# Optimization experiments

Hardware: AMD Instinct MI355X
Metric: run time of the kernel (lower is better)

## Reference

```python
import jax, jax.numpy as jnp
import numpy as np

B, T, D = 2, 2048, 2048
Q_HEADS, KV_HEADS, HEAD_DIM = 16, 4, 128
ROPE_BASE = 10000.0


def _apply_rotary(x_nhd, positions_n):
    # x_nhd: (N, H, head_dim); half-split rotary embedding.
    half = x_nhd.shape[-1] // 2
    inv_freq = 1.0 / (ROPE_BASE ** (jnp.arange(half, dtype=jnp.float32) / half))
    ang = positions_n.astype(jnp.float32)[:, None] * inv_freq  # (N, half)
    cos = jnp.cos(ang)[:, None, :]  # (N, 1, half)
    sin = jnp.sin(ang)[:, None, :]
    x1, x2 = x_nhd[..., :half], x_nhd[..., half:]
    return jnp.concatenate([x1 * cos - x2 * sin, x1 * sin + x2 * cos], axis=-1)


def setup_inputs() -> dict:
    key = jax.random.key(0)
    ks = jax.random.split(key, 5)
    s_in = 1.0 / np.sqrt(D)
    s_o = 1.0 / np.sqrt(Q_HEADS * HEAD_DIM)
    x = jax.random.normal(ks[0], (B, T, D), dtype=jnp.float32)
    positions = jnp.broadcast_to(jnp.arange(T, dtype=jnp.int32), (B, T))
    wq = jax.random.normal(ks[1], (Q_HEADS * HEAD_DIM, D), dtype=jnp.float32) * s_in
    wk = jax.random.normal(ks[2], (KV_HEADS * HEAD_DIM, D), dtype=jnp.float32) * s_in
    wv = jax.random.normal(ks[3], (KV_HEADS * HEAD_DIM, D), dtype=jnp.float32) * s_in
    wo = jax.random.normal(ks[4], (D, Q_HEADS * HEAD_DIM), dtype=jnp.float32) * s_o
    return {"x": x, "positions": positions, "wq": wq, "wk": wk, "wv": wv, "wo": wo}


def reference(x, positions, wq, wk, wv, wo):
    bsz, tsz, _ = x.shape
    q = jnp.einsum('btd,od->bto', x, wq).reshape(bsz, tsz, Q_HEADS, HEAD_DIM)
    k = jnp.einsum('btd,od->bto', x, wk).reshape(bsz, tsz, KV_HEADS, HEAD_DIM)
    v = jnp.einsum('btd,od->bto', x, wv).reshape(bsz, tsz, KV_HEADS, HEAD_DIM)
    pos_flat = positions.reshape(-1)
    q = _apply_rotary(q.reshape(-1, Q_HEADS, HEAD_DIM), pos_flat).reshape(bsz, tsz, Q_HEADS, HEAD_DIM)
    k = _apply_rotary(k.reshape(-1, KV_HEADS, HEAD_DIM), pos_flat).reshape(bsz, tsz, KV_HEADS, HEAD_DIM)
    rep = Q_HEADS // KV_HEADS
    k = jnp.repeat(k, rep, axis=2)
    v = jnp.repeat(v, rep, axis=2)
    logits = jnp.einsum('bthd,bThd->bhtT', q, k) / jnp.sqrt(jnp.float32(HEAD_DIM))
    causal = jnp.tril(jnp.ones((tsz, tsz), dtype=bool))
    logits = jnp.where(causal[None, None], logits, -1e9)
    weights = jax.nn.softmax(logits, axis=-1)
    ctx = jnp.einsum('bhtT,bThd->bthd', weights, v).reshape(bsz, tsz, Q_HEADS * HEAD_DIM)
    return jnp.einsum('bto,do->btd', ctx, wo)
```

## Files before the change

### kernel.cpp

```cpp
#include <hip/hip_runtime.h>
#include <hip/hip_bf16.h>

typedef __bf16 bf16x8 __attribute__((ext_vector_type(8)));
typedef float  f32x4  __attribute__((ext_vector_type(4)));
typedef float  f32x16 __attribute__((ext_vector_type(16)));
typedef unsigned int u32x2 __attribute__((ext_vector_type(2)));

#define B_   2
#define T_   2048
#define D_   2048
#define QH_  16
#define KVH_ 4
#define HD_  128
#define BT_  (B_ * T_)
#define KVD_ 512
#define SCL  0.12751744f

#define GLOAD_LDS16(g, l)                                        \
  __builtin_amdgcn_global_load_lds(                              \
      (const __attribute__((address_space(1))) void*)(g),        \
      (__attribute__((address_space(3))) void*)(l), 16, 0, 0)

#define SWZ(row)  ((((row) >> 3) ^ (row)) & 15)
#define SWZ8(row) ((((row) >> 3) ^ (row)) & 7)

__global__ __launch_bounds__(256) void cvt_all(
    const float* __restrict__ x, const float* __restrict__ wq,
    const float* __restrict__ wk, const float* __restrict__ wv,
    const float* __restrict__ wo, ushort* __restrict__ out) {
  const int i = blockIdx.x * 256 + threadIdx.x;
  int j = i;
  const float* src;
  float mul = 1.f;
  if (j < 2097152) { src = x; }
  else if ((j -= 2097152) < 1048576) { src = wq; mul = SCL; }
  else if ((j -= 1048576) < 262144)  { src = wk; }
  else if ((j -= 262144) < 262144)   { src = wv; }
  else { j -= 262144; src = wo; }
  float4 v = ((const float4*)src)[j];
  __hip_bfloat16 h0 = __float2bfloat16(v.x * mul);
  __hip_bfloat16 h1 = __float2bfloat16(v.y * mul);
  __hip_bfloat16 h2 = __float2bfloat16(v.z * mul);
  __hip_bfloat16 h3 = __float2bfloat16(v.w * mul);
  ushort4 o;
  o.x = *(ushort*)&h0; o.y = *(ushort*)&h1;
  o.z = *(ushort*)&h2; o.w = *(ushort*)&h3;
  ((ushort4*)out)[i] = o;
}

__global__ __launch_bounds__(256) void gemm_qkv(
    const ushort* __restrict__ X, const ushort* __restrict__ WQ,
    const ushort* __restrict__ WK, const ushort* __restrict__ WV,
    ushort* __restrict__ qo, ushort* __restrict__ ko, ushort* __restrict__ vo) {
  const int nb = blockIdx.x % 24;
  const int mb = blockIdx.x / 24;
  const int tid = threadIdx.x;
  const int wave = tid >> 6;
  const int lane = tid & 63;
  const int mrow = lane & 15;
  const int quad = lane >> 4;
  const int wm = wave >> 1;
  const int wn = wave & 1;
  const int m0 = mb * 128;
  const int K = D_;

  const ushort* Wg;
  if (nb < 16)      Wg = WQ + (size_t)nb * 128 * K;
  else if (nb < 20) Wg = WK + (size_t)(nb - 16) * 128 * K;
  else              Wg = WV + (size_t)(nb - 20) * 128 * K;

  __shared__ __align__(16) ushort At[2][128 * 64];
  __shared__ __align__(16) ushort Bt[2][128 * 64];

  f32x4 acc[4][4];
#pragma unroll
  for (int i = 0; i < 4; ++i)
#pragma unroll
    for (int j = 0; j < 4; ++j) acc[i][j] = (f32x4){0.f, 0.f, 0.f, 0.f};

  const ushort* Xg = X + (size_t)m0 * K;

  auto STAGE = [&](int buf, int k0) {
#pragma unroll
    for (int p = 0; p < 4; ++p) {
      const int c = p * 256 + tid;
      const int row = c >> 3;
      const int cc = (c & 7) ^ (row & 7);
      GLOAD_LDS16(Xg + (size_t)row * K + k0 + cc * 8,
                  At[buf] + (size_t)(p * 256 + wave * 64) * 8);
      GLOAD_LDS16(Wg + (size_t)row * K + k0 + cc * 8,
                  Bt[buf] + (size_t)(p * 256 + wave * 64) * 8);
    }
  };

  const int NT = K / 64;
  STAGE(0, 0);
  STAGE(1, 64);

  for (int t = 0; t < NT; ++t) {
    const int cur = t & 1;
    if (t + 2 < NT) asm volatile("s_waitcnt vmcnt(8)" ::: "memory");
    else            asm volatile("s_waitcnt vmcnt(0)" ::: "memory");
    __builtin_amdgcn_s_barrier();

    const ushort* Ac = At[cur];
    const ushort* Bc = Bt[cur];
#pragma unroll
    for (int s = 0; s < 2; ++s) {
      bf16x8 af[4], bfr[4];
#pragma unroll
      for (int mt = 0; mt < 4; ++mt) {
        const int row = wm * 64 + mt * 16 + mrow;
        af[mt] = *reinterpret_cast<const bf16x8*>(
            Ac + row * 64 + (((s * 4 + quad) ^ (row & 7)) * 8));
      }
#pragma unroll
      for (int nt = 0; nt < 4; ++nt) {
        const int row = wn * 64 + nt * 16 + mrow;
        bfr[nt] = *reinterpret_cast<const bf16x8*>(
            Bc + row * 64 + (((s * 4 + quad) ^ (row & 7)) * 8));
      }
#pragma unroll
      for (int mt = 0; mt < 4; ++mt)
#pragma unroll
        for (int nt = 0; nt < 4; ++nt)
          acc[mt][nt] = __builtin_amdgcn_mfma_f32_16x16x32_bf16(
              af[mt], bfr[nt], acc[mt][nt], 0, 0, 0);
    }

    asm volatile("s_waitcnt lgkmcnt(0)" ::: "memory");
    __builtin_amdgcn_s_barrier();
    if (t + 2 < NT) STAGE(cur, (t + 2) * 64);
  }

#pragma unroll
  for (int mt = 0; mt < 4; ++mt) {
#pragma unroll
    for (int nt = 0; nt < 4; ++nt) {
      const int colw = wn * 64 + nt * 16 + mrow;
      const int row0 = m0 + wm * 64 + mt * 16 + quad * 4;
      if (nb < 16) {
        const int col = nb * 128 + colw;
#pragma unroll
        for (int r = 0; r < 4; ++r) {
          __hip_bfloat16 hh = __float2bfloat16(acc[mt][nt][r]);
          qo[(size_t)(row0 + r) * 2048 + col] = *(ushort*)&hh;
        }
      } else if (nb < 20) {
        const int col = (nb - 16) * 128 + colw;
#pragma unroll
        for (int r = 0; r < 4; ++r) {
          __hip_bfloat16 hh = __float2bfloat16(acc[mt][nt][r]);
          ko[(size_t)(row0 + r) * KVD_ + col] = *(ushort*)&hh;
        }
      } else {
        const int col = (nb - 20) * 128 + colw;
        const int bb = row0 >> 11;
        const int t0 = row0 & (T_ - 1);
        ushort4 s4;
#pragma unroll
        for (int r = 0; r < 4; ++r) {
          __hip_bfloat16 hh = __float2bfloat16(acc[mt][nt][r]);
          (&s4.x)[r] = *(ushort*)&hh;
        }
        *(ushort4*)(vo + ((size_t)(bb * KVD_ + col)) * T_ + t0) = s4;
      }
    }
  }
}

__global__ __launch_bounds__(256) void gemm_o(
    const ushort* __restrict__ X, const ushort* __restrict__ W,
    float* __restrict__ Y, int M, int N, int K) {
  const int nb128 = N >> 7;
  const int mb = blockIdx.x / nb128;
  const int nb = blockIdx.x % nb128;
  const int tid = threadIdx.x;
  const int wave = tid >> 6;
  const int lane = tid & 63;
  const int mrow = lane & 15;
  const int quad = lane >> 4;
  const int wm = wave >> 1;
  const int wn = wave & 1;
  const int m0 = mb * 128;
  const int n0 = nb * 128;

  __shared__ __align__(16) ushort At[2][128 * 64];
  __shared__ __align__(16) ushort Bt[2][128 * 64];

  f32x4 acc[4][4];
#pragma unroll
  for (int i = 0; i < 4; ++i)
#pragma unroll
    for (int j = 0; j < 4; ++j) acc[i][j] = (f32x4){0.f, 0.f, 0.f, 0.f};

  const ushort* Xg = X + (size_t)m0 * K;
  const ushort* Wg = W + (size_t)n0 * K;

  auto STAGE = [&](int buf, int k0) {
#pragma unroll
    for (int p = 0; p < 4; ++p) {
      const int c = p * 256 + tid;
      const int row = c >> 3;
      const int cc = (c & 7) ^ (row & 7);
      GLOAD_LDS16(Xg + (size_t)row * K + k0 + cc * 8,
                  At[buf] + (size_t)(p * 256 + wave * 64) * 8);
      GLOAD_LDS16(Wg + (size_t)row * K + k0 + cc * 8,
                  Bt[buf] + (size_t)(p * 256 + wave * 64) * 8);
    }
  };

  const int NT = K / 64;
  STAGE(0, 0);
  STAGE(1, 64);

  for (int t = 0; t < NT; ++t) {
    const int cur = t & 1;
    if (t + 2 < NT) asm volatile("s_waitcnt vmcnt(8)" ::: "memory");
    else            asm volatile("s_waitcnt vmcnt(0)" ::: "memory");
    __builtin_amdgcn_s_barrier();

    const ushort* Ac = At[cur];
    const ushort* Bc = Bt[cur];
#pragma unroll
    for (int s = 0; s < 2; ++s) {
      bf16x8 af[4], bfr[4];
#pragma unroll
      for (int mt = 0; mt < 4; ++mt) {
        const int row = wm * 64 + mt * 16 + mrow;
        af[mt] = *reinterpret_cast<const bf16x8*>(
            Ac + row * 64 + (((s * 4 + quad) ^ (row & 7)) * 8));
      }
#pragma unroll
      for (int nt = 0; nt < 4; ++nt) {
        const int row = wn * 64 + nt * 16 + mrow;
        bfr[nt] = *reinterpret_cast<const bf16x8*>(
            Bc + row * 64 + (((s * 4 + quad) ^ (row & 7)) * 8));
      }
#pragma unroll
      for (int mt = 0; mt < 4; ++mt)
#pragma unroll
        for (int nt = 0; nt < 4; ++nt)
          acc[mt][nt] = __builtin_amdgcn_mfma_f32_16x16x32_bf16(
              af[mt], bfr[nt], acc[mt][nt], 0, 0, 0);
    }

    asm volatile("s_waitcnt lgkmcnt(0)" ::: "memory");
    __builtin_amdgcn_s_barrier();
    if (t + 2 < NT) STAGE(cur, (t + 2) * 64);
  }

#pragma unroll
  for (int mt = 0; mt < 4; ++mt)
#pragma unroll
    for (int nt = 0; nt < 4; ++nt) {
      const int col = n0 + wn * 64 + nt * 16 + mrow;
      const int row0 = m0 + wm * 64 + mt * 16 + quad * 4;
#pragma unroll
      for (int r = 0; r < 4; ++r)
        Y[(size_t)(row0 + r) * N + col] = acc[mt][nt][r];
    }
}

__global__ __launch_bounds__(256) void rope_kernel(
    __hip_bfloat16* __restrict__ q, __hip_bfloat16* __restrict__ k,
    const int* __restrict__ positions) {
  const int wave = threadIdx.x >> 6;
  const int lane = threadIdx.x & 63;
  const int p = blockIdx.x * 4 + wave;
  const int head = p % (QH_ + KVH_);
  const int bt = p / (QH_ + KVH_);

  __hip_bfloat16* base;
  if (head < QH_) base = q + ((size_t)bt * QH_ + head) * HD_;
  else            base = k + ((size_t)bt * KVH_ + (head - QH_)) * HD_;

  const float pos = (float)positions[bt];
  const float inv_freq = exp2f((float)lane * -0.20762050593f);
  const float ang = pos * inv_freq;
  const float c = cosf(ang);
  const float s = sinf(ang);

  const float x1 = __bfloat162float(base[lane]);
  const float x2 = __bfloat162float(base[lane + 64]);
  base[lane]      = __float2bfloat16(x1 * c - x2 * s);
  base[lane + 64] = __float2bfloat16(x1 * s + x2 * c);
}

static __device__ __forceinline__ unsigned pk2(float a, float b) {
  __hip_bfloat16 ha = __float2bfloat16(a);
  __hip_bfloat16 hb = __float2bfloat16(b);
  return (unsigned)(*(ushort*)&ha) | ((unsigned)(*(ushort*)&hb) << 16);
}

static __device__ __forceinline__ void hswap(unsigned& a, unsigned& b,
                                             const int hi) {
#if __has_builtin(__builtin_amdgcn_permlane32_swap)
  u32x2 r = __builtin_amdgcn_permlane32_swap(a, b, false, false);
  a = r.x;
  b = r.y;
#else
  unsigned s = __shfl_xor(hi ? a : b, 32, 64);
  unsigned na = hi ? s : a;
  b = hi ? b : s;
  a = na;
#endif
}

__global__ __launch_bounds__(256, 2) void attn_mfma(
    const ushort* __restrict__ q, const ushort* __restrict__ k,
    const ushort* __restrict__ vt, ushort* __restrict__ ctx) {
  const int tid = threadIdx.x;
  const int wave = tid >> 6;
  const int lane = tid & 63;
  const int m5 = lane & 31;
  const int hi = lane >> 5;
  const int parity = wave & 1;
  const int hh = wave >> 1;

  const int i = blockIdx.x;
  const int qt = i & 63;
  const int g  = i >> 6;
  const int b   = g >> 3;
  const int hkv = (g >> 1) & 3;
  const int hp  = g & 1;
  const int hq  = hkv * 4 + hp * 2 + hh;
  const int q0  = qt * 32;

  __shared__ __align__(16) ushort smem[16384];
  __shared__ float lbuf[2][32];
  ushort* kt   = smem;
  ushort* vtl  = smem + 8192;

  const ushort* qrow =
      q + ((size_t)(b * T_ + q0 + m5) * QH_ + hq) * HD_ + hi * 8;
  bf16x8 qf[8];
#pragma unroll
  for (int c = 0; c < 8; ++c)
    qf[c] = *reinterpret_cast<const bf16x8*>(qrow + c * 16);

  f32x16 o4[4];
#pragma unroll
  for (int dt = 0; dt < 4; ++dt)
#pragma unroll
    for (int r = 0; r < 16; ++r) o4[dt][r] = 0.f;
  float ls = 0.f;

  const ushort* kbase = k + ((size_t)b * T_ * KVH_ + hkv) * HD_;
  const ushort* vbase = vt + (size_t)(b * KVD_ + hkv * HD_) * T_;

  const int ns = (qt >> 1) + 1;

  for (int s = 0; s < ns; ++s) {
    const int j0 = s * 64;

#pragma unroll
    for (int p = 0; p < 4; ++p) {
      const int c = p * 256 + tid;
      const int krow = c >> 4;
      const int kco = (c & 15) ^ SWZ(krow);
      GLOAD_LDS16(kbase + (size_t)(j0 + krow) * KVD_ + kco * 8,
                  kt + (size_t)(p * 256 + wave * 64) * 8);
    }
#pragma unroll
    for (int p = 0; p < 4; ++p) {
      const int c = p * 256 + tid;
      const int vrow = c >> 3;
      const int vco = (c & 7) ^ SWZ8(vrow);
      GLOAD_LDS16(vbase + (size_t)vrow * T_ + j0 + vco * 8,
                  vtl + (size_t)(p * 256 + wave * 64) * 8);
    }
    asm volatile("s_waitcnt vmcnt(4)" ::: "memory");
    __builtin_amdgcn_s_barrier();

    const int c32 = 2 * s + parity;
    unsigned u0, u1, u2, u3, u4, u5, u6, u7;

    if (c32 <= qt) {
      __builtin_amdgcn_s_setprio(1);
      f32x16 sa;
#pragma unroll
      for (int r = 0; r < 16; ++r) sa[r] = 0.f;
      const int rowk = parity * 32 + m5;
#pragma unroll
      for (int c = 0; c < 8; ++c) {
        const int ch = (2 * c + hi) ^ SWZ(rowk);
        bf16x8 kf = *reinterpret_cast<const bf16x8*>(kt + rowk * 128 + ch * 8);
        sa = __builtin_amdgcn_mfma_f32_32x32x16_bf16(kf, qf[c], sa, 0, 0, 0);
      }

      float p[16];
      if (c32 == qt) {
#pragma unroll
        for (int r = 0; r < 16; ++r) {
          const int roff = (r & 3) + 8 * (r >> 2) + 4 * hi;
          p[r] = (roff > m5) ? 0.f : exp2f(sa[r]);
        }
      } else {
#pragma unroll
        for (int r = 0; r < 16; ++r) p[r] = exp2f(sa[r]);
      }
#pragma unroll
      for (int r = 0; r < 16; ++r) ls += p[r];

      u0 = pk2(p[0], p[1]);   u1 = pk2(p[2], p[3]);
      u2 = pk2(p[4], p[5]);   u3 = pk2(p[6], p[7]);
      u4 = pk2(p[8], p[9]);   u5 = pk2(p[10], p[11]);
      u6 = pk2(p[12], p[13]); u7 = pk2(p[14], p[15]);
      hswap(u0, u2, hi); hswap(u1, u3, hi);
      hswap(u4, u6, hi); hswap(u5, u7, hi);
      __builtin_amdgcn_s_setprio(0);
    }

    asm volatile("s_waitcnt vmcnt(0)" ::: "memory");
    __builtin_amdgcn_s_barrier();

    if (c32 <= qt) {
      __builtin_amdgcn_s_setprio(1);
#pragma unroll
      for (int half = 0; half < 2; ++half) {
        union { unsigned w[4]; bf16x8 v; } pa;
        pa.w[0] = half ? u4 : u0;
        pa.w[1] = half ? u5 : u1;
        pa.w[2] = half ? u6 : u2;
        pa.w[3] = half ? u7 : u3;
        const int gc2 = parity * 4 + half * 2;
#pragma unroll
        for (int dt = 0; dt < 4; ++dt) {
          const int rowv = dt * 32 + m5;
          const int chv = (gc2 + hi) ^ SWZ8(rowv);
          bf16x8 vf =
              *reinterpret_cast<const bf16x8*>(vtl + rowv * 64 + chv * 8);
          o4[dt] = __builtin_amdgcn_mfma_f32_32x32x16_bf16(pa.v, vf, o4[dt],
                                                           0, 0, 0);
        }
      }
      __builtin_amdgcn_s_setprio(0);
    }

    asm volatile("s_waitcnt lgkmcnt(0)" ::: "memory");
    __builtin_amdgcn_s_barrier();
  }

  const float lt = ls + __shfl_xor(ls, 32, 64);
  float* sO = (float*)smem;
  if (parity) {
#pragma unroll
    for (int reg = 0; reg < 16; ++reg) {
      const int qrw = (reg & 3) + 8 * (reg >> 2) + 4 * hi;
#pragma unroll
      for (int dt = 0; dt < 4; ++dt)
        sO[hh * 4096 + qrw * 128 + dt * 32 + m5] = o4[dt][reg];
    }
    if (hi == 0) lbuf[hh][m5] = lt;
  }
  __syncthreads();
  if (!parity) {
    const float ltot = lt + lbuf[hh][m5];
#pragma unroll
    for (int reg = 0; reg < 16; ++reg) {
      const int qrw = (reg & 3) + 8 * (reg >> 2) + 4 * hi;
      const float rl = 1.f / __shfl(ltot, qrw, 64);
      ushort* op =
          ctx + ((size_t)(b * T_ + q0 + qrw) * QH_ + hq) * HD_ + m5;
#pragma unroll
      for (int dt = 0; dt < 4; ++dt) {
        const float ov = o4[dt][reg] + sO[hh * 4096 + qrw * 128 + dt * 32 + m5];
        __hip_bfloat16 hb = __float2bfloat16(ov * rl);
        op[dt * 32] = *(ushort*)&hb;
      }
    }
  }
}

extern "C" void kernel_launch(void* const* d_in, const int* in_sizes, int n_in,
                              void* d_out, int out_size, void* d_ws, size_t ws_size,
                              hipStream_t stream) {
  const float* x  = (const float*)d_in[0];
  const int* pos  = (const int*)d_in[1];
  const float* wq = (const float*)d_in[2];
  const float* wk = (const float*)d_in[3];
  const float* wv = (const float*)d_in[4];
  const float* wo = (const float*)d_in[5];

  ushort* xb  = (ushort*)d_ws;
  ushort* wqb = xb  + (size_t)8388608;
  ushort* wkb = wqb + (size_t)4194304;
  ushort* wvb = wkb + (size_t)1048576;
  ushort* wob = wvb + (size_t)1048576;
  ushort* qb  = wob + (size_t)4194304;
  ushort* kb  = qb  + (size_t)8388608;
  ushort* vtb = kb  + (size_t)2097152;
  ushort* ctx = xb;

  cvt_all<<<18432, 256, 0, stream>>>(x, wq, wk, wv, wo, (ushort*)d_ws);

  gemm_qkv<<<(BT_ / 128) * 24, 256, 0, stream>>>(xb, wqb, wkb, wvb, qb, kb, vtb);

  rope_kernel<<<(BT_ * (QH_ + KVH_)) / 4, 256, 0, stream>>>(
      (__hip_bfloat16*)qb, (__hip_bfloat16*)kb, pos);

  attn_mfma<<<1024, 256, 0, stream>>>(qb, kb, vtb, ctx);

  gemm_o<<<(BT_ / 128) * (D_ / 128), 256, 0, stream>>>(
      ctx, wob, (float*)d_out, BT_, D_, QH_ * HD_);
}
```

Before: 331.9 us.

## Pair causal query tiles per block and double-buffer K/V staging in attention

Each attention block now handles two query tiles, a long one (63-pj) and a short one (pj), so the causal work per block is balanced. The grid is halved to 512 blocks. K/V tiles are double-buffered in LDS so the next tile's global-to-LDS load overlaps compute on the current one. The wait before the P·V step is removed. LDS doubles to 64KB per block, which may reduce occupancy, and fewer blocks may underfill the GPU.

```diff
diff --git a/kernel.cpp b/kernel.cpp
--- a/kernel.cpp
+++ b/kernel.cpp
@@ -318,158 +318,167 @@
   const int parity = wave & 1;
   const int hh = wave >> 1;
 
-  const int i = blockIdx.x;
-  const int qt = i & 63;
-  const int g  = i >> 6;
+  const int pj = blockIdx.x & 31;
+  const int g  = blockIdx.x >> 5;
   const int b   = g >> 3;
   const int hkv = (g >> 1) & 3;
   const int hp  = g & 1;
   const int hq  = hkv * 4 + hp * 2 + hh;
-  const int q0  = qt * 32;
-
-  __shared__ __align__(16) ushort smem[16384];
+
+  __shared__ __align__(16) ushort smem[32768];
   __shared__ float lbuf[2][32];
-  ushort* kt   = smem;
-  ushort* vtl  = smem + 8192;
-
-  const ushort* qrow =
-      q + ((size_t)(b * T_ + q0 + m5) * QH_ + hq) * HD_ + hi * 8;
-  bf16x8 qf[8];
-#pragma unroll
-  for (int c = 0; c < 8; ++c)
-    qf[c] = *reinterpret_cast<const bf16x8*>(qrow + c * 16);
-
-  f32x16 o4[4];
-#pragma unroll
-  for (int dt = 0; dt < 4; ++dt)
-#pragma unroll
-    for (int r = 0; r < 16; ++r) o4[dt][r] = 0.f;
-  float ls = 0.f;
 
   const ushort* kbase = k + ((size_t)b * T_ * KVH_ + hkv) * HD_;
   const ushort* vbase = vt + (size_t)(b * KVD_ + hkv * HD_) * T_;
 
-  const int ns = (qt >> 1) + 1;
-
-  for (int s = 0; s < ns; ++s) {
-    const int j0 = s * 64;
-
-#pragma unroll
-    for (int p = 0; p < 4; ++p) {
-      const int c = p * 256 + tid;
-      const int krow = c >> 4;
-      const int kco = (c & 15) ^ SWZ(krow);
-      GLOAD_LDS16(kbase + (size_t)(j0 + krow) * KVD_ + kco * 8,
-                  kt + (size_t)(p * 256 + wave * 64) * 8);
-    }
-#pragma unroll
-    for (int p = 0; p < 4; ++p) {
-      const int c = p * 256 + tid;
-      const int vrow = c >> 3;
-      const int vco = (c & 7) ^ SWZ8(vrow);
-      GLOAD_LDS16(vbase + (size_t)vrow * T_ + j0 + vco * 8,
-                  vtl + (size_t)(p * 256 + wave * 64) * 8);
-    }
-    asm volatile("s_waitcnt vmcnt(4)" ::: "memory");
-    __builtin_amdgcn_s_barrier();
-
-    const int c32 = 2 * s + parity;
-    unsigned u0, u1, u2, u3, u4, u5, u6, u7;
-
-    if (c32 <= qt) {
-      __builtin_amdgcn_s_setprio(1);
-      f32x16 sa;
-#pragma unroll
-      for (int r = 0; r < 16; ++r) sa[r] = 0.f;
-      const int rowk = parity * 32 + m5;
-#pragma unroll
-      for (int c = 0; c < 8; ++c) {
-        const int ch = (2 * c + hi) ^ SWZ(rowk);
-        bf16x8 kf = *reinterpret_cast<const bf16x8*>(kt + rowk * 128 + ch * 8);
-        sa = __builtin_amdgcn_mfma_f32_32x32x16_bf16(kf, qf[c], sa, 0, 0, 0);
-      }
-
-      float p[16];
-      if (c32 == qt) {
-#pragma unroll
-        for (int r = 0; r < 16; ++r) {
-          const int roff = (r & 3) + 8 * (r >> 2) + 4 * hi;
-          p[r] = (roff > m5) ? 0.f : exp2f(sa[r]);
-        }
+  for (int job = 0; job < 2; ++job) {
+    const int qt = job ? pj : 63 - pj;
+    const int q0 = qt * 32;
+    const int ns = (qt >> 1) + 1;
+
+    const ushort* qrow =
+        q + ((size_t)(b * T_ + q0 + m5) * QH_ + hq) * HD_ + hi * 8;
+    bf16x8 qf[8];
+#pragma unroll
+    for (int c = 0; c < 8; ++c)
+      qf[c] = *reinterpret_cast<const bf16x8*>(qrow + c * 16);
+
+    f32x16 o4[4];
+#pragma unroll
+    for (int dt = 0; dt < 4; ++dt)
+#pragma unroll
+      for (int r = 0; r < 16; ++r) o4[dt][r] = 0.f;
+    float ls = 0.f;
+
+    auto STAGE = [&](int buf, int s) {
+      const int j0 = s * 64;
+      ushort* kb_ = smem + buf * 16384;
+      ushort* vb_ = smem + buf * 16384 + 8192;
+#pragma unroll
+      for (int p = 0; p < 4; ++p) {
+        const int c = p * 256 + tid;
+        const int krow = c >> 4;
+        const int kco = (c & 15) ^ SWZ(krow);
+        GLOAD_LDS16(kbase + (size_t)(j0 + krow) * KVD_ + kco * 8,
+                    kb_ + (size_t)(p * 256 + wave * 64) * 8);
+      }
+#pragma unroll
+      for (int p = 0; p < 4; ++p) {
+        const int c = p * 256 + tid;
+        const int vrow = c >> 3;
+        const int vco = (c & 7) ^ SWZ8(vrow);
+        GLOAD_LDS16(vbase + (size_t)vrow * T_ + j0 + vco * 8,
+                    vb_ + (size_t)(p * 256 + wave * 64) * 8);
+      }
+    };
+
+    STAGE(0, 0);
+
+    for (int s = 0; s < ns; ++s) {
+      const int cur = s & 1;
+      if (s + 1 < ns) {
+        STAGE(cur ^ 1, s + 1);
+        asm volatile("s_waitcnt vmcnt(8)" ::: "memory");
       } else {
-#pragma unroll
-        for (int r = 0; r < 16; ++r) p[r] = exp2f(sa[r]);
-      }
-#pragma unroll
-      for (int r = 0; r < 16; ++r) ls += p[r];
-
-      u0 = pk2(p[0], p[1]);   u1 = pk2(p[2], p[3]);
-      u2 = pk2(p[4], p[5]);   u3 = pk2(p[6], p[7]);
-      u4 = pk2(p[8], p[9]);   u5 = pk2(p[10], p[11]);
-      u6 = pk2(p[12], p[13]); u7 = pk2(p[14], p[15]);
-      hswap(u0, u2, hi); hswap(u1, u3, hi);
-      hswap(u4, u6, hi); hswap(u5, u7, hi);
-      __builtin_amdgcn_s_setprio(0);
-    }
-
-    asm volatile("s_waitcnt vmcnt(0)" ::: "memory");
-    __builtin_amdgcn_s_barrier();
-
-    if (c32 <= qt) {
-      __builtin_amdgcn_s_setprio(1);
-#pragma unroll
-      for (int half = 0; half < 2; ++half) {
-        union { unsigned w[4]; bf16x8 v; } pa;
-        pa.w[0] = half ? u4 : u0;
-        pa.w[1] = half ? u5 : u1;
-        pa.w[2] = half ? u6 : u2;
-        pa.w[3] = half ? u7 : u3;
-        const int gc2 = parity * 4 + half * 2;
+        asm volatile("s_waitcnt vmcnt(0)" ::: "memory");
+      }
+      __builtin_amdgcn_s_barrier();
+
+      const ushort* kt  = smem + cur * 16384;
+      const ushort* vtl = smem + cur * 16384 + 8192;
+      const int c32 = 2 * s + parity;
+
+      if (c32 <= qt) {
+        __builtin_amdgcn_s_setprio(1);
+        f32x16 sa;
+#pragma unroll
+        for (int r = 0; r < 16; ++r) sa[r] = 0.f;
+        const int rowk = parity * 32 + m5;
+#pragma unroll
+        for (int c = 0; c < 8; ++c) {
+          const int ch = (2 * c + hi) ^ SWZ(rowk);
+          bf16x8 kf =
+              *reinterpret_cast<const bf16x8*>(kt + rowk * 128 + ch * 8);
+          sa = __builtin_amdgcn_mfma_f32_32x32x16_bf16(kf, qf[c], sa, 0, 0, 0);
+        }
+
+        float p[16];
+        if (c32 == qt) {
+#pragma unroll
+          for (int r = 0; r < 16; ++r) {
+            const int roff = (r & 3) + 8 * (r >> 2) + 4 * hi;
+            p[r] = (roff > m5) ? 0.f : exp2f(sa[r]);
+          }
+        } else {
+#pragma unroll
+          for (int r = 0; r < 16; ++r) p[r] = exp2f(sa[r]);
+        }
+#pragma unroll
+        for (int r = 0; r < 16; ++r) ls += p[r];
+
+        unsigned u0 = pk2(p[0], p[1]);   unsigned u1 = pk2(p[2], p[3]);
+        unsigned u2 = pk2(p[4], p[5]);   unsigned u3 = pk2(p[6], p[7]);
+        unsigned u4 = pk2(p[8], p[9]);   unsigned u5 = pk2(p[10], p[11]);
+        unsigned u6 = pk2(p[12], p[13]); unsigned u7 = pk2(p[14], p[15]);
+        hswap(u0, u2, hi); hswap(u1, u3, hi);
+        hswap(u4, u6, hi); hswap(u5, u7, hi);
+
+#pragma unroll
+        for (int half = 0; half < 2; ++half) {
+          union { unsigned w[4]; bf16x8 v; } pa;
+          pa.w[0] = half ? u4 : u0;
+          pa.w[1] = half ? u5 : u1;
+          pa.w[2] = half ? u6 : u2;
+          pa.w[3] = half ? u7 : u3;
+          const int gc2 = parity * 4 + half * 2;
+#pragma unroll
+          for (int dt = 0; dt < 4; ++dt) {
+            const int rowv = dt * 32 + m5;
+            const int chv = (gc2 + hi) ^ SWZ8(rowv);
+            bf16x8 vf =
+                *reinterpret_cast<const bf16x8*>(vtl + rowv * 64 + chv * 8);
+            o4[dt] = __builtin_amdgcn_mfma_f32_32x32x16_bf16(pa.v, vf, o4[dt],
+                                                             0, 0, 0);
+          }
+        }
+        __builtin_amdgcn_s_setprio(0);
+      }
+
+      asm volatile("s_waitcnt lgkmcnt(0)" ::: "memory");
+      __builtin_amdgcn_s_barrier();
+    }
+
+    const float lt = ls + __shfl_xor(ls, 32, 64);
+    float* sO = (float*)smem;
+    if (parity) {
+#pragma unroll
+      for (int reg = 0; reg < 16; ++reg) {
+        const int qrw = (reg & 3) + 8 * (reg >> 2) + 4 * hi;
+#pragma unroll
+        for (int dt = 0; dt < 4; ++dt)
+          sO[hh * 4096 + qrw * 128 + dt * 32 + m5] = o4[dt][reg];
+      }
+      if (hi == 0) lbuf[hh][m5] = lt;
+    }
+    __syncthreads();
+    if (!parity) {
+      const float ltot = lt + lbuf[hh][m5];
+#pragma unroll
+      for (int reg = 0; reg < 16; ++reg) {
+        const int qrw = (reg & 3) + 8 * (reg >> 2) + 4 * hi;
+        const float rl = 1.f / __shfl(ltot, qrw, 64);
+        ushort* op =
+            ctx + ((size_t)(b * T_ + q0 + qrw) * QH_ + hq) * HD_ + m5;
 #pragma unroll
         for (int dt = 0; dt < 4; ++dt) {
-          const int rowv = dt * 32 + m5;
-          const int chv = (gc2 + hi) ^ SWZ8(rowv);
-          bf16x8 vf =
-              *reinterpret_cast<const bf16x8*>(vtl + rowv * 64 + chv * 8);
-          o4[dt] = __builtin_amdgcn_mfma_f32_32x32x16_bf16(pa.v, vf, o4[dt],
-                                                           0, 0, 0);
-        }
-      }
-      __builtin_amdgcn_s_setprio(0);
-    }
-
-    asm volatile("s_waitcnt lgkmcnt(0)" ::: "memory");
-    __builtin_amdgcn_s_barrier();
-  }
-
-  const float lt = ls + __shfl_xor(ls, 32, 64);
-  float* sO = (float*)smem;
-  if (parity) {
-#pragma unroll
-    for (int reg = 0; reg < 16; ++reg) {
-      const int qrw = (reg & 3) + 8 * (reg >> 2) + 4 * hi;
-#pragma unroll
-      for (int dt = 0; dt < 4; ++dt)
-        sO[hh * 4096 + qrw * 128 + dt * 32 + m5] = o4[dt][reg];
-    }
-    if (hi == 0) lbuf[hh][m5] = lt;
-  }
-  __syncthreads();
-  if (!parity) {
-    const float ltot = lt + lbuf[hh][m5];
-#pragma unroll
-    for (int reg = 0; reg < 16; ++reg) {
-      const int qrw = (reg & 3) + 8 * (reg >> 2) + 4 * hi;
-      const float rl = 1.f / __shfl(ltot, qrw, 64);
-      ushort* op =
-          ctx + ((size_t)(b * T_ + q0 + qrw) * QH_ + hq) * HD_ + m5;
-#pragma unroll
-      for (int dt = 0; dt < 4; ++dt) {
-        const float ov = o4[dt][reg] + sO[hh * 4096 + qrw * 128 + dt * 32 + m5];
-        __hip_bfloat16 hb = __float2bfloat16(ov * rl);
-        op[dt * 32] = *(ushort*)&hb;
-      }
-    }
+          const float ov =
+              o4[dt][reg] + sO[hh * 4096 + qrw * 128 + dt * 32 + m5];
+          __hip_bfloat16 hb = __float2bfloat16(ov * rl);
+          op[dt * 32] = *(ushort*)&hb;
+        }
+      }
+    }
+    __syncthreads();
   }
 }
 
@@ -500,7 +509,7 @@
   rope_kernel<<<(BT_ * (QH_ + KVH_)) / 4, 256, 0, stream>>>(
       (__hip_bfloat16*)qb, (__hip_bfloat16*)kb, pos);
 
-  attn_mfma<<<1024, 256, 0, stream>>>(qb, kb, vtb, ctx);
+  attn_mfma<<<512, 256, 0, stream>>>(qb, kb, vtb, ctx);
 
   gemm_o<<<(BT_ / 128) * (D_ / 128), 256, 0, stream>>>(
       ctx, wob, (float*)d_out, BT_, D_, QH_ * HD_);
```

Measured after the change: 298.4 us. 1.11x faster.
